# Kernel tuning notes

Measured on AMD Instinct MI355X. Metric: run time of the kernel, lower is better.

## Reference

```python
import jax, jax.numpy as jnp
import numpy as np

B, S, DIM = 2, 2048, 2048
H, DK, DR, DC, DCP, DV = 16, 128, 64, 512, 1024, 128


def setup_inputs() -> dict:
    key = jax.random.key(0)
    ks = jax.random.split(key, 8)
    s = 0.02  # weight init scale
    return {
        "x": jax.random.normal(ks[0], (B, S, DIM), jnp.float32),
        "W_c": jax.random.normal(ks[1], (DIM, DC), jnp.float32) * s,
        "W_c_prime": jax.random.normal(ks[2], (DIM, DCP), jnp.float32) * s,
        "W_qc": jax.random.normal(ks[3], (H, DCP, DK), jnp.float32) * s,
        "W_qr": jax.random.normal(ks[4], (H, DCP, DR), jnp.float32) * s,
        "W_kc": jax.random.normal(ks[5], (H, DC, DK), jnp.float32) * s,
        "W_kr": jax.random.normal(ks[6], (DIM, DR), jnp.float32) * s,
        "W_v": jax.random.normal(ks[7], (H, DC, DV), jnp.float32) * s,
    }


def reference(x, W_c, W_c_prime, W_qc, W_qr, W_kc, W_kr, W_v):
    # Latent compressions
    c = x @ W_c                 # [B,S,DC]  compressed KV latent
    cp = x @ W_c_prime          # [B,S,DCP] compressed Q latent
    # Per-head projections, vectorized over heads
    q_c = jnp.einsum('bsc,hck->bhsk', cp, W_qc)   # [B,H,S,DK]
    q_r = jnp.einsum('bsc,hcr->bhsr', cp, W_qr)   # [B,H,S,DR]
    k_c = jnp.einsum('bsc,hck->bhsk', c, W_kc)    # [B,H,S,DK]
    k_r = x @ W_kr                                 # [B,S,DR] shared across heads
    q = jnp.concatenate([q_c, q_r], axis=-1)                               # [B,H,S,DK+DR]
    k = jnp.concatenate([k_c, jnp.broadcast_to(k_r[:, None], (B, H, S, DR))], axis=-1)
    scale = 1.0 / np.sqrt(DK + DR)
    scores = jnp.einsum('bhsd,bhtd->bhst', q, k) * scale                   # [B,H,S,S]
    causal = jnp.tril(jnp.ones((S, S), dtype=bool))
    scores = jnp.where(causal, scores, -jnp.inf)
    probs = jax.nn.softmax(scores.astype(jnp.float32), axis=-1).astype(q.dtype)
    v = jnp.einsum('bsc,hcv->bhsv', c, W_v)                                # [B,H,S,DV]
    out = jnp.einsum('bhst,bhtv->bhsv', probs, v)                          # [B,H,S,DV]
    return out.transpose(0, 2, 1, 3).reshape(B, S, H * DV)                 # concat heads
```

## Files before the change

kernel.cpp:

```cpp
#include <hip/hip_runtime.h>
#include <stdint.h>

typedef __bf16 bf16;
typedef __bf16 bfx8 __attribute__((ext_vector_type(8)));
typedef __bf16 bfx4 __attribute__((ext_vector_type(4)));
typedef float floatx4 __attribute__((ext_vector_type(4)));

#define B_ 2
#define S_ 2048
#define DIM_ 2048
#define H_ 16
#define DK_ 128
#define DR_ 64
#define DC_ 512
#define DCP_ 1024
#define DV_ 128
#define DQK_ 192

#define MASK_VAL (-30000.0f)
#define C1_ 0.10411754f

__global__ void k_cast(const float* __restrict__ in, bf16* __restrict__ out) {
    size_t i = ((size_t)blockIdx.x * 256 + threadIdx.x) * 8;
    float4 a = *(const float4*)(in + i);
    float4 b = *(const float4*)(in + i + 4);
    bfx8 r;
    r[0] = (bf16)a.x; r[1] = (bf16)a.y; r[2] = (bf16)a.z; r[3] = (bf16)a.w;
    r[4] = (bf16)b.x; r[5] = (bf16)b.y; r[6] = (bf16)b.z; r[7] = (bf16)b.w;
    *(bfx8*)(out + i) = r;
}

__global__ void k_transpose(const float* __restrict__ in, bf16* __restrict__ out,
                            int K, int N) {
    __shared__ float tile[32][33];
    int h = blockIdx.z;
    int n0 = blockIdx.x * 32, k0 = blockIdx.y * 32;
    const float* ip = in + (size_t)h * K * N;
    bf16* op = out + (size_t)h * K * N;
    int tx = threadIdx.x & 31, ty = threadIdx.x >> 5;
#pragma unroll
    for (int i = 0; i < 32; i += 8)
        tile[ty + i][tx] = ip[(size_t)(k0 + ty + i) * N + (n0 + tx)];
    __syncthreads();
#pragma unroll
    for (int i = 0; i < 32; i += 8)
        op[(size_t)(n0 + ty + i) * K + (k0 + tx)] = (bf16)tile[tx][ty + i];
}

__device__ __forceinline__ void gld16(const bf16* g, bf16* l) {
    __builtin_amdgcn_global_load_lds(
        (const __attribute__((address_space(1))) void*)g,
        (__attribute__((address_space(3))) void*)l, 16, 0, 0);
}

__device__ __forceinline__ bfx8 frag_ld(const bf16* lds, int row, int quad) {
    int pb = quad ^ ((row >> 1) & 3);
    return *(const bfx8*)(lds + row * 32 + pb * 8);
}

__device__ __forceinline__ void gemm_core(const bf16* __restrict__ A,
                                          const bf16* __restrict__ Bt,
                                          int K, int rowlimB,
                                          floatx4 acc[4][4],
                                          bf16* A_lds, bf16* B_lds) {
    int tid = threadIdx.x, wave = tid >> 6, lane = tid & 63;
    int l15 = lane & 15, quad = lane >> 4;
    int wm = (wave & 1) * 64, wn = (wave >> 1) * 64;
    int ch0 = wave * 2, ch1 = wave * 2 + 1;
    int r0 = ch0 * 16 + (lane >> 2), r1 = ch1 * 16 + (lane >> 2);
    int kb0 = (lane & 3) ^ ((r0 >> 1) & 3), kb1 = (lane & 3) ^ ((r1 >> 1) & 3);
    int rb0 = r0 <= rowlimB ? r0 : rowlimB;
    int rb1 = r1 <= rowlimB ? r1 : rowlimB;
    const bf16* a0 = A + (size_t)r0 * K + kb0 * 8;
    const bf16* a1 = A + (size_t)r1 * K + kb1 * 8;
    const bf16* b0 = Bt + (size_t)rb0 * K + kb0 * 8;
    const bf16* b1 = Bt + (size_t)rb1 * K + kb1 * 8;
    bf16* da0 = A_lds + ch0 * 512;
    bf16* da1 = A_lds + ch1 * 512;
    bf16* db0 = B_lds + ch0 * 512;
    bf16* db1 = B_lds + ch1 * 512;
    for (int k0 = 0; k0 < K; k0 += 32) {
        __syncthreads();
        gld16(a0 + k0, da0);
        gld16(a1 + k0, da1);
        gld16(b0 + k0, db0);
        gld16(b1 + k0, db1);
        __syncthreads();
        bfx8 a[4], b[4];
#pragma unroll
        for (int t = 0; t < 4; ++t) a[t] = frag_ld(A_lds, wm + t * 16 + l15, quad);
#pragma unroll
        for (int t = 0; t < 4; ++t) b[t] = frag_ld(B_lds, wn + t * 16 + l15, quad);
#pragma unroll
        for (int mt = 0; mt < 4; ++mt)
#pragma unroll
            for (int nt = 0; nt < 4; ++nt)
                acc[mt][nt] = __builtin_amdgcn_mfma_f32_16x16x32_bf16(
                    a[mt], b[nt], acc[mt][nt], 0, 0, 0);
    }
}

__global__ __launch_bounds__(256, 3) void k_gemm1(
    const bf16* __restrict__ xb, const bf16* __restrict__ Wt_c,
    const bf16* __restrict__ Wt_cp, const bf16* __restrict__ Wt_kr,
    bf16* __restrict__ c_ws, bf16* __restrict__ cp_ws, bf16* __restrict__ kr_ws) {
    __shared__ __attribute__((aligned(16))) bf16 A_lds[128 * 32];
    __shared__ __attribute__((aligned(16))) bf16 B_lds[128 * 32];
    int bx = blockIdx.x, by = blockIdx.y;
    const bf16* Bt; bf16* outp; int ldc, col0, rowlim;
    if (bx < 4)       { Bt = Wt_c  + (size_t)bx * 128 * DIM_;       outp = c_ws;  ldc = DC_;  col0 = bx * 128;       rowlim = 127; }
    else if (bx < 12) { Bt = Wt_cp + (size_t)(bx - 4) * 128 * DIM_; outp = cp_ws; ldc = DCP_; col0 = (bx - 4) * 128; rowlim = 127; }
    else              { Bt = Wt_kr;                                  outp = kr_ws; ldc = DR_;  col0 = 0;              rowlim = 63;  }
    floatx4 acc[4][4];
#pragma unroll
    for (int i = 0; i < 4; ++i)
#pragma unroll
        for (int j = 0; j < 4; ++j) acc[i][j] = (floatx4){0.f, 0.f, 0.f, 0.f};
    gemm_core(xb + (size_t)by * 128 * DIM_, Bt, DIM_, rowlim, acc, A_lds, B_lds);
    int tid = threadIdx.x, wave = tid >> 6, lane = tid & 63;
    int l15 = lane & 15, quad = lane >> 4;
    int wm = (wave & 1) * 64, wn = (wave >> 1) * 64;
#pragma unroll
    for (int mt = 0; mt < 4; ++mt)
#pragma unroll
        for (int nt = 0; nt < 4; ++nt) {
            int n = wn + nt * 16 + l15;
            if (n > rowlim) continue;
#pragma unroll
            for (int r = 0; r < 4; ++r) {
                int m = by * 128 + wm + mt * 16 + quad * 4 + r;
                outp[(size_t)m * ldc + col0 + n] = (bf16)acc[mt][nt][r];
            }
        }
}

__global__ __launch_bounds__(256, 3) void k_gemm2(
    const bf16* __restrict__ cp_ws, const bf16* __restrict__ Wt_qc,
    const bf16* __restrict__ Wt_qr, bf16* __restrict__ q_ws) {
    __shared__ __attribute__((aligned(16))) bf16 A_lds[128 * 32];
    __shared__ __attribute__((aligned(16))) bf16 B_lds[128 * 32];
    int bx = blockIdx.x, by = blockIdx.y, h = blockIdx.z;
    const bf16* Bt; int col0, rowlim;
    if (bx == 0) { Bt = Wt_qc + (size_t)h * DK_ * DCP_; col0 = 0;   rowlim = 127; }
    else         { Bt = Wt_qr + (size_t)h * DR_ * DCP_; col0 = 128; rowlim = 63;  }
    floatx4 acc[4][4];
#pragma unroll
    for (int i = 0; i < 4; ++i)
#pragma unroll
        for (int j = 0; j < 4; ++j) acc[i][j] = (floatx4){0.f, 0.f, 0.f, 0.f};
    gemm_core(cp_ws + (size_t)by * 128 * DCP_, Bt, DCP_, rowlim, acc, A_lds, B_lds);
    int tid = threadIdx.x, wave = tid >> 6, lane = tid & 63;
    int l15 = lane & 15, quad = lane >> 4;
    int wm = (wave & 1) * 64, wn = (wave >> 1) * 64;
#pragma unroll
    for (int mt = 0; mt < 4; ++mt)
#pragma unroll
        for (int nt = 0; nt < 4; ++nt) {
            int n = wn + nt * 16 + l15;
            if (n > rowlim) continue;
#pragma unroll
            for (int r = 0; r < 4; ++r) {
                int m = by * 128 + wm + mt * 16 + quad * 4 + r;
                int b = m >> 11, s = m & 2047;
                q_ws[(((size_t)b * H_ + h) * S_ + s) * DQK_ + col0 + n] =
                    (bf16)(acc[mt][nt][r] * C1_);
            }
        }
}

__global__ __launch_bounds__(256, 3) void k_gemm3(
    const bf16* __restrict__ c_ws, const bf16* __restrict__ Wt_kc,
    const bf16* __restrict__ Wt_v, bf16* __restrict__ kc_ws, bf16* __restrict__ vt_ws) {
    __shared__ __attribute__((aligned(16))) bf16 A_lds[128 * 32];
    __shared__ __attribute__((aligned(16))) bf16 B_lds[128 * 32];
    int bx = blockIdx.x, by = blockIdx.y, h = blockIdx.z;
    const bf16* Bt = (bx == 0) ? (Wt_kc + (size_t)h * DK_ * DC_)
                               : (Wt_v  + (size_t)h * DV_ * DC_);
    floatx4 acc[4][4];
#pragma unroll
    for (int i = 0; i < 4; ++i)
#pragma unroll
        for (int j = 0; j < 4; ++j) acc[i][j] = (floatx4){0.f, 0.f, 0.f, 0.f};
    gemm_core(c_ws + (size_t)by * 128 * DC_, Bt, DC_, 127, acc, A_lds, B_lds);
    int tid = threadIdx.x, wave = tid >> 6, lane = tid & 63;
    int l15 = lane & 15, quad = lane >> 4;
    int wm = (wave & 1) * 64, wn = (wave >> 1) * 64;
#pragma unroll
    for (int mt = 0; mt < 4; ++mt)
#pragma unroll
        for (int nt = 0; nt < 4; ++nt) {
            int n = wn + nt * 16 + l15;
            if (bx == 0) {
#pragma unroll
                for (int r = 0; r < 4; ++r) {
                    int m = by * 128 + wm + mt * 16 + quad * 4 + r;
                    int b = m >> 11, s = m & 2047;
                    kc_ws[(((size_t)b * H_ + h) * S_ + s) * DK_ + n] = (bf16)acc[mt][nt][r];
                }
            } else {
                int m0 = by * 128 + wm + mt * 16 + quad * 4;
                int b = m0 >> 11, s = m0 & 2047;
                bfx4 pack;
#pragma unroll
                for (int r = 0; r < 4; ++r) pack[r] = (bf16)acc[mt][nt][r];
                *(bfx4*)(&vt_ws[(((size_t)b * H_ + h) * DV_ + n) * S_ + s]) = pack;
            }
        }
}

#define KSTR 200
#define VSTR 72
#define PSTR 68

__global__ __launch_bounds__(256, 1) void k_attn(
    const bf16* __restrict__ q_ws, const bf16* __restrict__ kc_ws,
    const bf16* __restrict__ kr_ws, const bf16* __restrict__ vt_ws,
    float* __restrict__ out) {
    __shared__ __attribute__((aligned(16))) bf16 K_lds[64 * KSTR];
    __shared__ __attribute__((aligned(16))) bf16 V_lds[128 * VSTR];
    __shared__ __attribute__((aligned(16))) bf16 P_lds[128 * PSTR];
    int p = blockIdx.x;
    int bh = blockIdx.y, b = bh >> 4, h = bh & 15;
    int tid = threadIdx.x, wave = tid >> 6, lane = tid & 63;
    int l15 = lane & 15, quad = lane >> 4;

    bf16 ov = (bf16)(l15 == 0 ? 1.f : 0.f);
    bfx8 ones8 = {ov, ov, ov, ov, ov, ov, ov, ov};

    int kn[4], kcc[4], rn[2], rcc[2], vr[4], vcc[4];
#pragma unroll
    for (int i = 0; i < 4; ++i) { int f = (i * 256 + tid) * 8; kn[i] = f >> 7; kcc[i] = f & 127; }
#pragma unroll
    for (int i = 0; i < 2; ++i) { int f = (i * 256 + tid) * 8; rn[i] = f >> 6; rcc[i] = f & 63; }
#pragma unroll
    for (int i = 0; i < 4; ++i) { int f = (i * 256 + tid) * 8; vr[i] = f >> 6; vcc[i] = f & 63; }
    const bf16* kcp[4]; const bf16* krp[2]; const bf16* vp[4];
#pragma unroll
    for (int i = 0; i < 4; ++i) kcp[i] = kc_ws + ((size_t)bh * S_ + kn[i]) * DK_ + kcc[i];
#pragma unroll
    for (int i = 0; i < 2; ++i) krp[i] = kr_ws + ((size_t)b * S_ + rn[i]) * DR_ + rcc[i];
#pragma unroll
    for (int i = 0; i < 4; ++i) vp[i] = vt_ws + ((size_t)bh * DV_ + vr[i]) * S_ + vcc[i];

    for (int ph = 0; ph < 2; ++ph) {
        int qt = ph ? p : 15 - p;
        int q0 = qt * 128, ntiles = 2 * qt + 2;

        bfx8 qf[2][6];
#pragma unroll
        for (int mt = 0; mt < 2; ++mt) {
            const bf16* qrow =
                q_ws + ((size_t)bh * S_ + q0 + wave * 32 + mt * 16 + l15) * DQK_;
#pragma unroll
            for (int ks = 0; ks < 6; ++ks)
                qf[mt][ks] = *(const bfx8*)(qrow + ks * 32 + quad * 8);
        }

        floatx4 o_acc[2][9];
#pragma unroll
        for (int mt = 0; mt < 2; ++mt)
#pragma unroll
            for (int vt = 0; vt < 9; ++vt) o_acc[mt][vt] = (floatx4){0.f, 0.f, 0.f, 0.f};

        bfx8 pk[4], pr[2], pv[4];
#pragma unroll
        for (int i = 0; i < 4; ++i) pk[i] = *(const bfx8*)(kcp[i]);
#pragma unroll
        for (int i = 0; i < 2; ++i) pr[i] = *(const bfx8*)(krp[i]);
#pragma unroll
        for (int i = 0; i < 4; ++i) pv[i] = *(const bfx8*)(vp[i]);

        for (int t = 0; t < ntiles; ++t) {
            __syncthreads();
#pragma unroll
            for (int i = 0; i < 4; ++i) *(bfx8*)(&K_lds[kn[i] * KSTR + kcc[i]]) = pk[i];
#pragma unroll
            for (int i = 0; i < 2; ++i) *(bfx8*)(&K_lds[rn[i] * KSTR + 128 + rcc[i]]) = pr[i];
#pragma unroll
            for (int i = 0; i < 4; ++i) *(bfx8*)(&V_lds[vr[i] * VSTR + vcc[i]]) = pv[i];
            __syncthreads();
            if (t + 1 < ntiles) {
                size_t kv1 = (size_t)(t + 1) * 64;
#pragma unroll
                for (int i = 0; i < 4; ++i) pk[i] = *(const bfx8*)(kcp[i] + kv1 * DK_);
#pragma unroll
                for (int i = 0; i < 2; ++i) pr[i] = *(const bfx8*)(krp[i] + kv1 * DR_);
#pragma unroll
                for (int i = 0; i < 4; ++i) pv[i] = *(const bfx8*)(vp[i] + kv1);
            }
            floatx4 sc[2][4];
#pragma unroll
            for (int mt = 0; mt < 2; ++mt)
#pragma unroll
                for (int nt = 0; nt < 4; ++nt) sc[mt][nt] = (floatx4){0.f, 0.f, 0.f, 0.f};
#pragma unroll
            for (int ks = 0; ks < 6; ++ks)
#pragma unroll
                for (int nt = 0; nt < 4; ++nt) {
                    bfx8 kf = *(const bfx8*)(&K_lds[(nt * 16 + l15) * KSTR + ks * 32 + quad * 8]);
                    sc[0][nt] = __builtin_amdgcn_mfma_f32_16x16x32_bf16(qf[0][ks], kf, sc[0][nt], 0, 0, 0);
                    sc[1][nt] = __builtin_amdgcn_mfma_f32_16x16x32_bf16(qf[1][ks], kf, sc[1][nt], 0, 0, 0);
                }
            if (t >= ntiles - 2) {
                int kv0 = t * 64;
#pragma unroll
                for (int mt = 0; mt < 2; ++mt)
#pragma unroll
                    for (int nt = 0; nt < 4; ++nt)
#pragma unroll
                        for (int r = 0; r < 4; ++r) {
                            int n_g = kv0 + nt * 16 + l15;
                            int q_g = q0 + wave * 32 + mt * 16 + quad * 4 + r;
                            if (n_g > q_g) sc[mt][nt][r] = MASK_VAL;
                        }
            }
#pragma unroll
            for (int mt = 0; mt < 2; ++mt)
#pragma unroll
                for (int nt = 0; nt < 4; ++nt)
#pragma unroll
                    for (int r = 0; r < 4; ++r)
                        P_lds[(wave * 32 + mt * 16 + quad * 4 + r) * PSTR + nt * 16 + l15] =
                            (bf16)exp2f(sc[mt][nt][r]);
#pragma unroll
            for (int ks2 = 0; ks2 < 2; ++ks2) {
                bfx8 pf0 = *(const bfx8*)(&P_lds[(wave * 32 + l15) * PSTR + ks2 * 32 + quad * 8]);
                bfx8 pf1 = *(const bfx8*)(&P_lds[(wave * 32 + 16 + l15) * PSTR + ks2 * 32 + quad * 8]);
#pragma unroll
                for (int vt = 0; vt < 8; ++vt) {
                    bfx8 vf = *(const bfx8*)(&V_lds[(vt * 16 + l15) * VSTR + ks2 * 32 + quad * 8]);
                    o_acc[0][vt] = __builtin_amdgcn_mfma_f32_16x16x32_bf16(pf0, vf, o_acc[0][vt], 0, 0, 0);
                    o_acc[1][vt] = __builtin_amdgcn_mfma_f32_16x16x32_bf16(pf1, vf, o_acc[1][vt], 0, 0, 0);
                }
                o_acc[0][8] = __builtin_amdgcn_mfma_f32_16x16x32_bf16(pf0, ones8, o_acc[0][8], 0, 0, 0);
                o_acc[1][8] = __builtin_amdgcn_mfma_f32_16x16x32_bf16(pf1, ones8, o_acc[1][8], 0, 0, 0);
            }
        }
#pragma unroll
        for (int mt = 0; mt < 2; ++mt) {
            float rinv[4];
#pragma unroll
            for (int r = 0; r < 4; ++r)
                rinv[r] = 1.f / __shfl(o_acc[mt][8][r], lane & 48);
#pragma unroll
            for (int vt = 0; vt < 8; ++vt)
#pragma unroll
                for (int r = 0; r < 4; ++r) {
                    int s = q0 + wave * 32 + mt * 16 + quad * 4 + r;
                    int v = vt * 16 + l15;
                    out[((size_t)b * S_ + s) * (H_ * DV_) + h * DV_ + v] =
                        o_acc[mt][vt][r] * rinv[r];
                }
        }
    }
}

extern "C" void kernel_launch(void* const* d_in, const int* in_sizes, int n_in,
                              void* d_out, int out_size, void* d_ws, size_t ws_size,
                              hipStream_t stream) {
    const float* x    = (const float*)d_in[0];
    const float* W_c  = (const float*)d_in[1];
    const float* W_cp = (const float*)d_in[2];
    const float* W_qc = (const float*)d_in[3];
    const float* W_qr = (const float*)d_in[4];
    const float* W_kc = (const float*)d_in[5];
    const float* W_kr = (const float*)d_in[6];
    const float* W_v  = (const float*)d_in[7];
    float* out = (float*)d_out;

    bf16* c_ws  = (bf16*)d_out;
    bf16* cp_ws = c_ws + (size_t)B_ * S_ * DC_;
    bf16* xb    = cp_ws + (size_t)B_ * S_ * DCP_;

    char* ws = (char*)d_ws;
    size_t off = 0;
    auto alloc = [&](size_t elems) { bf16* p = (bf16*)(ws + off); off += elems * sizeof(bf16); return p; };
    bf16* Wt_c  = alloc((size_t)DIM_ * DC_);
    bf16* Wt_cp = alloc((size_t)DIM_ * DCP_);
    bf16* Wt_qc = alloc((size_t)H_ * DCP_ * DK_);
    bf16* Wt_qr = alloc((size_t)H_ * DCP_ * DR_);
    bf16* Wt_kc = alloc((size_t)H_ * DC_ * DK_);
    bf16* Wt_kr = alloc((size_t)DIM_ * DR_);
    bf16* Wt_v  = alloc((size_t)H_ * DC_ * DV_);
    bf16* kr_ws = alloc((size_t)B_ * S_ * DR_);
    bf16* q_ws  = alloc((size_t)B_ * H_ * S_ * DQK_);
    bf16* kc_ws = alloc((size_t)B_ * H_ * S_ * DK_);
    bf16* vt_ws = alloc((size_t)B_ * H_ * DV_ * S_);

    k_cast<<<dim3(4096), 256, 0, stream>>>(x, xb);
    k_transpose<<<dim3(DC_ / 32, DIM_ / 32, 1),  256, 0, stream>>>(W_c,  Wt_c,  DIM_, DC_);
    k_transpose<<<dim3(DCP_ / 32, DIM_ / 32, 1), 256, 0, stream>>>(W_cp, Wt_cp, DIM_, DCP_);
    k_transpose<<<dim3(DK_ / 32, DCP_ / 32, H_), 256, 0, stream>>>(W_qc, Wt_qc, DCP_, DK_);
    k_transpose<<<dim3(DR_ / 32, DCP_ / 32, H_), 256, 0, stream>>>(W_qr, Wt_qr, DCP_, DR_);
    k_transpose<<<dim3(DK_ / 32, DC_ / 32, H_),  256, 0, stream>>>(W_kc, Wt_kc, DC_, DK_);
    k_transpose<<<dim3(DR_ / 32, DIM_ / 32, 1),  256, 0, stream>>>(W_kr, Wt_kr, DIM_, DR_);
    k_transpose<<<dim3(DV_ / 32, DC_ / 32, H_),  256, 0, stream>>>(W_v,  Wt_v,  DC_, DV_);

    k_gemm1<<<dim3(13, 32), 256, 0, stream>>>(xb, Wt_c, Wt_cp, Wt_kr, c_ws, cp_ws, kr_ws);
    k_gemm2<<<dim3(2, 32, H_), 256, 0, stream>>>(cp_ws, Wt_qc, Wt_qr, q_ws);
    k_gemm3<<<dim3(2, 32, H_), 256, 0, stream>>>(c_ws, Wt_kc, Wt_v, kc_ws, vt_ws);
    k_attn<<<dim3(8, B_ * H_), 256, 0, stream>>>(q_ws, kc_ws, kr_ws, vt_ws, out);
}
```

Measured before the change: 332.8 us.

## Split attention KV loop across two wave groups and combine partial outputs in LDS

After: 348.1 us. +4.6%, slower.

```diff
diff --git a/kernel.cpp b/kernel.cpp
--- a/kernel.cpp
+++ b/kernel.cpp
@@ -211,29 +211,39 @@
 #define KSTR 200
 #define VSTR 72
 #define PSTR 68
-
-__global__ __launch_bounds__(256, 1) void k_attn(
+#define KB_ (64 * KSTR * 2)
+#define VB_ (128 * VSTR * 2)
+#define PB_ (128 * PSTR * 2)
+#define GB_ (KB_ + VB_ + PB_)
+#define OSTR 132
+
+__global__ __launch_bounds__(512, 2) void k_attn(
     const bf16* __restrict__ q_ws, const bf16* __restrict__ kc_ws,
     const bf16* __restrict__ kr_ws, const bf16* __restrict__ vt_ws,
     float* __restrict__ out) {
-    __shared__ __attribute__((aligned(16))) bf16 K_lds[64 * KSTR];
-    __shared__ __attribute__((aligned(16))) bf16 V_lds[128 * VSTR];
-    __shared__ __attribute__((aligned(16))) bf16 P_lds[128 * PSTR];
+    __shared__ __attribute__((aligned(16))) char smem[2 * GB_];
     int p = blockIdx.x;
     int bh = blockIdx.y, b = bh >> 4, h = bh & 15;
     int tid = threadIdx.x, wave = tid >> 6, lane = tid & 63;
+    int grp = wave >> 2, wv = wave & 3, gtid = tid & 255;
     int l15 = lane & 15, quad = lane >> 4;
+
+    bf16* K_lds = (bf16*)(smem + grp * GB_);
+    bf16* V_lds = (bf16*)(smem + grp * GB_ + KB_);
+    bf16* P_lds = (bf16*)(smem + grp * GB_ + KB_ + VB_);
+    float* Ocmb = (float*)smem;
+    float* Lcmb = (float*)(smem + 128 * OSTR * 4);
 
     bf16 ov = (bf16)(l15 == 0 ? 1.f : 0.f);
     bfx8 ones8 = {ov, ov, ov, ov, ov, ov, ov, ov};
 
     int kn[4], kcc[4], rn[2], rcc[2], vr[4], vcc[4];
 #pragma unroll
-    for (int i = 0; i < 4; ++i) { int f = (i * 256 + tid) * 8; kn[i] = f >> 7; kcc[i] = f & 127; }
-#pragma unroll
-    for (int i = 0; i < 2; ++i) { int f = (i * 256 + tid) * 8; rn[i] = f >> 6; rcc[i] = f & 63; }
-#pragma unroll
-    for (int i = 0; i < 4; ++i) { int f = (i * 256 + tid) * 8; vr[i] = f >> 6; vcc[i] = f & 63; }
+    for (int i = 0; i < 4; ++i) { int f = (i * 256 + gtid) * 8; kn[i] = f >> 7; kcc[i] = f & 127; }
+#pragma unroll
+    for (int i = 0; i < 2; ++i) { int f = (i * 256 + gtid) * 8; rn[i] = f >> 6; rcc[i] = f & 63; }
+#pragma unroll
+    for (int i = 0; i < 4; ++i) { int f = (i * 256 + gtid) * 8; vr[i] = f >> 6; vcc[i] = f & 63; }
     const bf16* kcp[4]; const bf16* krp[2]; const bf16* vp[4];
 #pragma unroll
     for (int i = 0; i < 4; ++i) kcp[i] = kc_ws + ((size_t)bh * S_ + kn[i]) * DK_ + kcc[i];
@@ -244,13 +254,13 @@
 
     for (int ph = 0; ph < 2; ++ph) {
         int qt = ph ? p : 15 - p;
-        int q0 = qt * 128, ntiles = 2 * qt + 2;
+        int q0 = qt * 128, niter = qt + 1;
 
         bfx8 qf[2][6];
 #pragma unroll
         for (int mt = 0; mt < 2; ++mt) {
             const bf16* qrow =
-                q_ws + ((size_t)bh * S_ + q0 + wave * 32 + mt * 16 + l15) * DQK_;
+                q_ws + ((size_t)bh * S_ + q0 + wv * 32 + mt * 16 + l15) * DQK_;
 #pragma unroll
             for (int ks = 0; ks < 6; ++ks)
                 qf[mt][ks] = *(const bfx8*)(qrow + ks * 32 + quad * 8);
@@ -263,14 +273,17 @@
             for (int vt = 0; vt < 9; ++vt) o_acc[mt][vt] = (floatx4){0.f, 0.f, 0.f, 0.f};
 
         bfx8 pk[4], pr[2], pv[4];
-#pragma unroll
-        for (int i = 0; i < 4; ++i) pk[i] = *(const bfx8*)(kcp[i]);
-#pragma unroll
-        for (int i = 0; i < 2; ++i) pr[i] = *(const bfx8*)(krp[i]);
-#pragma unroll
-        for (int i = 0; i < 4; ++i) pv[i] = *(const bfx8*)(vp[i]);
-
-        for (int t = 0; t < ntiles; ++t) {
+        {
+            size_t kv = (size_t)grp * 64;
+#pragma unroll
+            for (int i = 0; i < 4; ++i) pk[i] = *(const bfx8*)(kcp[i] + kv * DK_);
+#pragma unroll
+            for (int i = 0; i < 2; ++i) pr[i] = *(const bfx8*)(krp[i] + kv * DR_);
+#pragma unroll
+            for (int i = 0; i < 4; ++i) pv[i] = *(const bfx8*)(vp[i] + kv);
+        }
+
+        for (int it = 0; it < niter; ++it) {
             __syncthreads();
 #pragma unroll
             for (int i = 0; i < 4; ++i) *(bfx8*)(&K_lds[kn[i] * KSTR + kcc[i]]) = pk[i];
@@ -279,8 +292,8 @@
 #pragma unroll
             for (int i = 0; i < 4; ++i) *(bfx8*)(&V_lds[vr[i] * VSTR + vcc[i]]) = pv[i];
             __syncthreads();
-            if (t + 1 < ntiles) {
-                size_t kv1 = (size_t)(t + 1) * 64;
+            if (it + 1 < niter) {
+                size_t kv1 = (size_t)(2 * (it + 1) + grp) * 64;
 #pragma unroll
                 for (int i = 0; i < 4; ++i) pk[i] = *(const bfx8*)(kcp[i] + kv1 * DK_);
 #pragma unroll
@@ -301,8 +314,8 @@
                     sc[0][nt] = __builtin_amdgcn_mfma_f32_16x16x32_bf16(qf[0][ks], kf, sc[0][nt], 0, 0, 0);
                     sc[1][nt] = __builtin_amdgcn_mfma_f32_16x16x32_bf16(qf[1][ks], kf, sc[1][nt], 0, 0, 0);
                 }
-            if (t >= ntiles - 2) {
-                int kv0 = t * 64;
+            if (it == niter - 1) {
+                int kv0 = (2 * it + grp) * 64;
 #pragma unroll
                 for (int mt = 0; mt < 2; ++mt)
 #pragma unroll
@@ -310,7 +323,7 @@
 #pragma unroll
                         for (int r = 0; r < 4; ++r) {
                             int n_g = kv0 + nt * 16 + l15;
-                            int q_g = q0 + wave * 32 + mt * 16 + quad * 4 + r;
+                            int q_g = q0 + wv * 32 + mt * 16 + quad * 4 + r;
                             if (n_g > q_g) sc[mt][nt][r] = MASK_VAL;
                         }
             }
@@ -320,12 +333,12 @@
                 for (int nt = 0; nt < 4; ++nt)
 #pragma unroll
                     for (int r = 0; r < 4; ++r)
-                        P_lds[(wave * 32 + mt * 16 + quad * 4 + r) * PSTR + nt * 16 + l15] =
+                        P_lds[(wv * 32 + mt * 16 + quad * 4 + r) * PSTR + nt * 16 + l15] =
                             (bf16)exp2f(sc[mt][nt][r]);
 #pragma unroll
             for (int ks2 = 0; ks2 < 2; ++ks2) {
-                bfx8 pf0 = *(const bfx8*)(&P_lds[(wave * 32 + l15) * PSTR + ks2 * 32 + quad * 8]);
-                bfx8 pf1 = *(const bfx8*)(&P_lds[(wave * 32 + 16 + l15) * PSTR + ks2 * 32 + quad * 8]);
+                bfx8 pf0 = *(const bfx8*)(&P_lds[(wv * 32 + l15) * PSTR + ks2 * 32 + quad * 8]);
+                bfx8 pf1 = *(const bfx8*)(&P_lds[(wv * 32 + 16 + l15) * PSTR + ks2 * 32 + quad * 8]);
 #pragma unroll
                 for (int vt = 0; vt < 8; ++vt) {
                     bfx8 vf = *(const bfx8*)(&V_lds[(vt * 16 + l15) * VSTR + ks2 * 32 + quad * 8]);
@@ -336,21 +349,46 @@
                 o_acc[1][8] = __builtin_amdgcn_mfma_f32_16x16x32_bf16(pf1, ones8, o_acc[1][8], 0, 0, 0);
             }
         }
-#pragma unroll
-        for (int mt = 0; mt < 2; ++mt) {
-            float rinv[4];
-#pragma unroll
-            for (int r = 0; r < 4; ++r)
-                rinv[r] = 1.f / __shfl(o_acc[mt][8][r], lane & 48);
-#pragma unroll
-            for (int vt = 0; vt < 8; ++vt)
-#pragma unroll
-                for (int r = 0; r < 4; ++r) {
-                    int s = q0 + wave * 32 + mt * 16 + quad * 4 + r;
-                    int v = vt * 16 + l15;
-                    out[((size_t)b * S_ + s) * (H_ * DV_) + h * DV_ + v] =
-                        o_acc[mt][vt][r] * rinv[r];
-                }
+
+        __syncthreads();
+        if (grp == 1) {
+#pragma unroll
+            for (int mt = 0; mt < 2; ++mt) {
+#pragma unroll
+                for (int vt = 0; vt < 8; ++vt)
+#pragma unroll
+                    for (int r = 0; r < 4; ++r)
+                        Ocmb[(wv * 32 + mt * 16 + quad * 4 + r) * OSTR + vt * 16 + l15] =
+                            o_acc[mt][vt][r];
+                if (l15 == 0)
+#pragma unroll
+                    for (int r = 0; r < 4; ++r)
+                        Lcmb[wv * 32 + mt * 16 + quad * 4 + r] = o_acc[mt][8][r];
+            }
+        }
+        __syncthreads();
+        if (grp == 0) {
+#pragma unroll
+            for (int mt = 0; mt < 2; ++mt) {
+                if (l15 == 0)
+#pragma unroll
+                    for (int r = 0; r < 4; ++r)
+                        o_acc[mt][8][r] += Lcmb[wv * 32 + mt * 16 + quad * 4 + r];
+                float rinv[4];
+#pragma unroll
+                for (int r = 0; r < 4; ++r)
+                    rinv[r] = 1.f / __shfl(o_acc[mt][8][r], lane & 48);
+#pragma unroll
+                for (int vt = 0; vt < 8; ++vt)
+#pragma unroll
+                    for (int r = 0; r < 4; ++r) {
+                        int row = wv * 32 + mt * 16 + quad * 4 + r;
+                        int s = q0 + row;
+                        int v = vt * 16 + l15;
+                        out[((size_t)b * S_ + s) * (H_ * DV_) + h * DV_ + v] =
+                            (o_acc[mt][vt][r] + Ocmb[row * OSTR + v]) * rinv[r];
+                    }
+            }
         }
     }
 }
@@ -399,5 +437,5 @@
     k_gemm1<<<dim3(13, 32), 256, 0, stream>>>(xb, Wt_c, Wt_cp, Wt_kr, c_ws, cp_ws, kr_ws);
     k_gemm2<<<dim3(2, 32, H_), 256, 0, stream>>>(cp_ws, Wt_qc, Wt_qr, q_ws);
     k_gemm3<<<dim3(2, 32, H_), 256, 0, stream>>>(c_ws, Wt_kc, Wt_v, kc_ws, vt_ws);
-    k_attn<<<dim3(8, B_ * H_), 256, 0, stream>>>(q_ws, kc_ws, kr_ws, vt_ws, out);
-}
+    k_attn<<<dim3(8, B_ * H_), 512, 0, stream>>>(q_ws, kc_ws, kr_ws, vt_ws, out);
+}
```
